# Performance work log

Measured on AMD Instinct MI355X. Metric: run time of the kernel, lower is better.

## Reference

```python
import jax, jax.numpy as jnp
import numpy as np

D_MODEL, N_LEVELS, N_HEADS, N_POINTS = 256, 4, 8, 4
HEAD_DIM = D_MODEL // N_HEADS
SPATIAL = np.array([[128, 128], [64, 64], [32, 32], [16, 16]], dtype=np.int64)
STARTS = np.concatenate([[0], np.cumsum(SPATIAL[:, 0] * SPATIAL[:, 1])[:-1]]).astype(np.int64)
N_TOK = int((SPATIAL[:, 0] * SPATIAL[:, 1]).sum())  # 21760
B, NQ = 2, 8192


def setup_inputs() -> dict:
    key = jax.random.key(0)
    ks = jax.random.split(key, 12)
    s = 1.0 / np.sqrt(D_MODEL)
    return {
        "query": jax.random.normal(ks[0], (B, NQ, D_MODEL), jnp.float32),
        "reference_points": jax.random.uniform(ks[1], (B, NQ, N_LEVELS, 2), jnp.float32),
        "input_flatten": jax.random.normal(ks[2], (B, N_TOK, D_MODEL), jnp.float32),
        "input_spatial_shapes": jnp.asarray(SPATIAL),
        "input_level_start_index": jnp.asarray(STARTS),
        "Wq": jax.random.normal(ks[3], (D_MODEL, D_MODEL), jnp.float32) * s,
        "bq": jnp.zeros((D_MODEL,), jnp.float32),
        "Wv": jax.random.normal(ks[4], (D_MODEL, D_MODEL), jnp.float32) * s,
        "bv": jnp.zeros((D_MODEL,), jnp.float32),
        "Wa": jax.random.normal(ks[5], (D_MODEL, N_HEADS * N_LEVELS * N_POINTS), jnp.float32) * s,
        "ba": jnp.zeros((N_HEADS * N_LEVELS * N_POINTS,), jnp.float32),
        "sampling_loc": jax.random.uniform(ks[6], (N_HEADS, N_LEVELS, N_POINTS, 2), jnp.float32, -0.1, 0.1),
        "Wo": jax.random.normal(ks[7], (D_MODEL, D_MODEL), jnp.float32) * s,
        "bo": jnp.zeros((D_MODEL,), jnp.float32),
    }


def _bilinear_sample(v_flat, grid, Hl, Wl):
    # v_flat: [B, H, Hl*Wl, Dh]; grid: [B, Nq, H, P, 2] in [-1, 1]
    b, nq, h, p, _ = grid.shape
    gx, gy = grid[..., 0], grid[..., 1]
    # align_corners=False pixel coordinates
    ix = ((gx + 1.0) * Wl - 1.0) * 0.5
    iy = ((gy + 1.0) * Hl - 1.0) * 0.5
    x0f, y0f = jnp.floor(ix), jnp.floor(iy)
    x0, y0 = x0f.astype(jnp.int32), y0f.astype(jnp.int32)
    x1, y1 = x0 + 1, y0 + 1
    wx1, wy1 = ix - x0f, iy - y0f
    wx0, wy0 = 1.0 - wx1, 1.0 - wy1

    def t(a):  # [B,Nq,H,P] -> [B,H,Nq*P]
        return a.transpose(0, 2, 1, 3).reshape(b, h, nq * p)

    def corner(yi, xi, w):
        valid = (xi >= 0) & (xi < Wl) & (yi >= 0) & (yi < Hl)
        idx = jnp.clip(yi, 0, Hl - 1) * Wl + jnp.clip(xi, 0, Wl - 1)
        g = jnp.take_along_axis(v_flat, t(idx)[..., None], axis=2)  # [B,H,Nq*P,Dh]
        return g * t(w * valid.astype(w.dtype))[..., None]

    out = (corner(y0, x0, wy0 * wx0) + corner(y0, x1, wy0 * wx1)
           + corner(y1, x0, wy1 * wx0) + corner(y1, x1, wy1 * wx1))
    return out.reshape(b, h, nq, p, -1)  # [B,H,Nq,P,Dh]


def reference(query, reference_points, input_flatten, input_spatial_shapes,
              input_level_start_index, Wq, bq, Wv, bv, Wa, ba, sampling_loc, Wo, bo):
    b, nq, c = query.shape
    h, L, p, _ = sampling_loc.shape
    dh = c // h
    q = query @ Wq + bq                                   # [B,Nq,C]
    attn = (q @ Wa + ba).reshape(b, nq, h, L, p)
    attn = jax.nn.softmax(attn, axis=-1)                  # softmax over points per level
    v = (input_flatten @ Wv + bv).reshape(b, -1, h, dh)   # [B,N,H,Dh]
    loc = reference_points[:, :, None, :, None, :] + sampling_loc[None, None]  # [B,Nq,H,L,P,2]
    grid = 2.0 * loc - 1.0
    shapes = np.asarray(input_spatial_shapes)
    starts = np.asarray(input_level_start_index)
    samples = []
    for lvl in range(L):
        Hl, Wl = int(shapes[lvl, 0]), int(shapes[lvl, 1])
        s0 = int(starts[lvl])
        vl = v[:, s0:s0 + Hl * Wl].transpose(0, 2, 1, 3)  # [B,H,Hl*Wl,Dh]
        samples.append(_bilinear_sample(vl, grid[:, :, :, lvl], Hl, Wl))
    samples = jnp.stack(samples, axis=3)                  # [B,H,Nq,L,P,Dh]
    out = jnp.einsum('bhnlpd,bnhlp->bnhd', samples, attn).reshape(b, nq, c)
    return out @ Wo + bo
```

## Files before the change

kernel.cpp:

```cpp
#include <hip/hip_runtime.h>
#include <hip/hip_bf16.h>

#define BATCH 2
#define NQ 8192
#define NTOK 21760

typedef __attribute__((ext_vector_type(4))) float f32x4;
typedef __attribute__((ext_vector_type(8))) short s16x8;

static __device__ __forceinline__ unsigned short f2bu(float x) {
    __hip_bfloat16 h = __float2bfloat16(x);
    return __builtin_bit_cast(unsigned short, h);
}
static __device__ __forceinline__ float blo(unsigned int u) { return __uint_as_float(u << 16); }
static __device__ __forceinline__ float bhi(unsigned int u) { return __uint_as_float(u & 0xffff0000u); }

__global__ void wqa_kernel(const float* __restrict__ Wq, const float* __restrict__ Wa,
                           const float* __restrict__ bq, const float* __restrict__ ba,
                           unsigned short* __restrict__ WqaT, float* __restrict__ bqa) {
    const int i = blockIdx.x;
    const int j = threadIdx.x;
    float acc = 0.f;
#pragma unroll 8
    for (int k = 0; k < 256; ++k) acc += Wq[i * 256 + k] * Wa[k * 128 + j];
    WqaT[j * 256 + i] = f2bu(acc);
    if (i == 0) {
        float b = ba[j];
#pragma unroll 8
        for (int k = 0; k < 256; ++k) b += bq[k] * Wa[k * 128 + j];
        bqa[j] = b;
    }
}

__global__ __launch_bounds__(256) void transpose_kernel(const float* __restrict__ Wv, const float* __restrict__ Wo,
                                                        unsigned short* __restrict__ WvT, unsigned short* __restrict__ WoT) {
    __shared__ float t[32][33];
    const int bid = blockIdx.x;
    const int mat = bid >> 6;
    const int tile = bid & 63;
    const int i0 = (tile >> 3) * 32, j0 = (tile & 7) * 32;
    const float* src = mat ? Wo : Wv;
    unsigned short* dst = mat ? WoT : WvT;
    const int tx = threadIdx.x & 31, ty = threadIdx.x >> 5;
#pragma unroll
    for (int r = 0; r < 4; ++r)
        t[ty + 8 * r][tx] = src[(i0 + ty + 8 * r) * 256 + j0 + tx];
    __syncthreads();
#pragma unroll
    for (int r = 0; r < 4; ++r)
        dst[(j0 + ty + 8 * r) * 256 + i0 + tx] = f2bu(t[tx][ty + 8 * r]);
}

template <int BM, int BN, int WRN, int WCN, bool AFP32, bool BF16OUT>
__global__ __launch_bounds__(256) void gemm_mfma(
    const void* __restrict__ Av, const unsigned short* __restrict__ Bt,
    const float* __restrict__ bias, void* __restrict__ Cv, int N) {
    constexpr int K = 256, NT = 4;
    constexpr int IM = BM / (WRN * 16);
    constexpr int JN = BN / (WCN * 16);
    constexpr int RA = BM / 32;
    constexpr int RB = BN / 32;
    __shared__ __align__(16) char As[BM * 128];
    __shared__ __align__(16) char Bs[BN * 128];
    const int tid = threadIdx.x;
    const int lane = tid & 63;
    const int wave = tid >> 6;
    const int wr = wave / WCN, wc = wave % WCN;
    const int bm = blockIdx.y * BM, bn = blockIdx.x * BN;
    const int srow = tid >> 3;
    const int skc = (tid & 7) * 8;

    f32x4 acc[IM][JN] = {};
    float4 af0[2][RA], af1[2][RA];
    s16x8 ab[2][RA], bb[2][RB];

    auto loadT = [&](int t, int buf) {
        const int k0 = t * 64;
#pragma unroll
        for (int r = 0; r < RA; ++r) {
            const int row = bm + srow + r * 32;
            if constexpr (AFP32) {
                const float* Af = (const float*)Av + (size_t)row * K + k0 + skc;
                af0[buf][r] = *(const float4*)Af;
                af1[buf][r] = *(const float4*)(Af + 4);
            } else {
                ab[buf][r] = *(const s16x8*)((const unsigned short*)Av + (size_t)row * K + k0 + skc);
            }
        }
#pragma unroll
        for (int r = 0; r < RB; ++r) {
            const int row = bn + srow + r * 32;
            bb[buf][r] = *(const s16x8*)(Bt + (size_t)row * K + k0 + skc);
        }
    };
    auto writeT = [&](int buf) {
#pragma unroll
        for (int r = 0; r < RA; ++r) {
            const int row = srow + r * 32;
            const int byte = (row * 128 + skc * 2) ^ ((row & 7) << 4);
            s16x8 av;
            if constexpr (AFP32) {
                const float4 f0 = af0[buf][r], f1 = af1[buf][r];
                av[0] = (short)f2bu(f0.x); av[1] = (short)f2bu(f0.y);
                av[2] = (short)f2bu(f0.z); av[3] = (short)f2bu(f0.w);
                av[4] = (short)f2bu(f1.x); av[5] = (short)f2bu(f1.y);
                av[6] = (short)f2bu(f1.z); av[7] = (short)f2bu(f1.w);
            } else {
                av = ab[buf][r];
            }
            *(s16x8*)(As + byte) = av;
        }
#pragma unroll
        for (int r = 0; r < RB; ++r) {
            const int row = srow + r * 32;
            const int byte = (row * 128 + skc * 2) ^ ((row & 7) << 4);
            *(s16x8*)(Bs + byte) = bb[buf][r];
        }
    };

    loadT(0, 0);
#pragma unroll
    for (int t = 0; t < NT; ++t) {
        if (t) __syncthreads();
        writeT(t & 1);
        if (t + 1 < NT) loadT(t + 1, (t + 1) & 1);
        __syncthreads();
#pragma unroll
        for (int f = 0; f < 2; ++f) {
            s16x8 a[IM], b[JN];
#pragma unroll
            for (int i = 0; i < IM; ++i) {
                const int arow = wr * (IM * 16) + i * 16 + (lane & 15);
                const int abyte = (arow * 128 + f * 64 + (lane >> 4) * 16) ^ ((arow & 7) << 4);
                a[i] = *(const s16x8*)(As + abyte);
            }
#pragma unroll
            for (int j = 0; j < JN; ++j) {
                const int brow = wc * (JN * 16) + j * 16 + (lane & 15);
                const int bbyte = (brow * 128 + f * 64 + (lane >> 4) * 16) ^ ((brow & 7) << 4);
                b[j] = *(const s16x8*)(Bs + bbyte);
            }
#pragma unroll
            for (int i = 0; i < IM; ++i)
#pragma unroll
                for (int j = 0; j < JN; ++j)
                    acc[i][j] = __builtin_amdgcn_mfma_f32_16x16x32_bf16(a[i], b[j], acc[i][j], 0, 0, 0);
        }
    }

#pragma unroll
    for (int i = 0; i < IM; ++i) {
        const int row0 = bm + wr * (IM * 16) + i * 16 + (lane >> 4) * 4;
#pragma unroll
        for (int j = 0; j < JN; ++j) {
            const int col = bn + wc * (JN * 16) + j * 16 + (lane & 15);
            const float bsv = bias[col];
#pragma unroll
            for (int q = 0; q < 4; ++q) {
                const float val = acc[i][j][q] + bsv;
                if constexpr (BF16OUT)
                    ((unsigned short*)Cv)[(size_t)(row0 + q) * N + col] = f2bu(val);
                else
                    ((float*)Cv)[(size_t)(row0 + q) * N + col] = val;
            }
        }
    }
}

__global__ __launch_bounds__(256) void sample_kernel(
    const float* __restrict__ refp, const float* __restrict__ sloc,
    const unsigned int* __restrict__ v,
    const float* __restrict__ logits,
    unsigned int* __restrict__ samp) {
    const int tid = threadIdx.x;
    const int q0 = blockIdx.x * 4;
    __shared__ int4 metaI[512];
    __shared__ float4 metaW[512];
    __shared__ float slc[256];
    __shared__ float lgs[512];
    __shared__ float rps[32];

    {
        const int l = (tid >> 3) & 3;
        slc[tid] = sloc[tid] * (float)(128 >> l) - 0.5f;
    }
    lgs[tid] = logits[(size_t)q0 * 128 + tid];
    lgs[tid + 256] = logits[(size_t)q0 * 128 + tid + 256];
    if (tid < 32) rps[tid] = refp[(size_t)q0 * 8 + tid];
    __syncthreads();

#pragma unroll
    for (int ss = 0; ss < 2; ++ss) {
        const int h = tid & 7;
        const int p = (tid >> 3) & 3;
        const int l = (tid >> 5) & 3;
        const int qi = (tid >> 7) + ss * 2;
        const int lp = l * 4 + p;
        const int bq = q0 + qi;
        const int b = bq >> 13;
        const int Wl = 128 >> l;
        const float lg = lgs[qi * 128 + h * 16 + lp];
        float m = fmaxf(lg, __shfl_xor(lg, 8));
        m = fmaxf(m, __shfl_xor(m, 16));
        const float e = __expf(lg - m);
        float sum = e + __shfl_xor(e, 8);
        sum += __shfl_xor(sum, 16);
        const float a = e / sum;
        const float fW = (float)Wl;
        const float ix = fmaf(rps[qi * 8 + l * 2 + 0], fW, slc[h * 32 + l * 8 + p * 2 + 0]);
        const float iy = fmaf(rps[qi * 8 + l * 2 + 1], fW, slc[h * 32 + l * 8 + p * 2 + 1]);
        const float xf = floorf(ix), yf = floorf(iy);
        const int x0 = (int)xf, y0 = (int)yf;
        const int x1 = x0 + 1, y1 = y0 + 1;
        float wx1 = ix - xf, wy1 = iy - yf;
        float wx0 = 1.f - wx1, wy0 = 1.f - wy1;
        wx0 = ((unsigned)x0 < (unsigned)Wl) ? wx0 : 0.f;
        wx1 = ((unsigned)x1 < (unsigned)Wl) ? wx1 : 0.f;
        wy0 = ((unsigned)y0 < (unsigned)Wl) ? wy0 * a : 0.f;
        wy1 = ((unsigned)y1 < (unsigned)Wl) ? wy1 * a : 0.f;
        const int x0c = min(max(x0, 0), Wl - 1);
        const int x1c = min(max(x1, 0), Wl - 1);
        const int y0c = min(max(y0, 0), Wl - 1);
        const int y1c = min(max(y1, 0), Wl - 1);
        const int SS = (65536 - (65536 >> (2 * l))) / 3;
        const int base = b * (NTOK * 128) + SS * 128 + h * 16;
        const int r0 = y0c * Wl, r1 = y1c * Wl;
        const int s = lp * 32 + qi * 8 + h;
        metaI[s] = make_int4(base + (r0 + x0c) * 128, base + (r0 + x1c) * 128,
                             base + (r1 + x0c) * 128, base + (r1 + x1c) * 128);
        metaW[s] = make_float4(wy0 * wx0, wy0 * wx1, wy1 * wx0, wy1 * wx1);
    }
    __syncthreads();

    const int qi = tid >> 6, h = (tid >> 3) & 7, c = tid & 7;
    const unsigned int* vp = v + c * 2;
    float a0 = 0.f, a1 = 0.f, a2 = 0.f, a3 = 0.f;
#pragma unroll
    for (int lp = 0; lp < 16; ++lp) {
        const int s = lp * 32 + qi * 8 + h;
        const int4 I = metaI[s];
        const float4 W = metaW[s];
        uint2 u;
        u = *(const uint2*)(vp + I.x);
        a0 = fmaf(blo(u.x), W.x, a0); a1 = fmaf(bhi(u.x), W.x, a1);
        a2 = fmaf(blo(u.y), W.x, a2); a3 = fmaf(bhi(u.y), W.x, a3);
        u = *(const uint2*)(vp + I.y);
        a0 = fmaf(blo(u.x), W.y, a0); a1 = fmaf(bhi(u.x), W.y, a1);
        a2 = fmaf(blo(u.y), W.y, a2); a3 = fmaf(bhi(u.y), W.y, a3);
        u = *(const uint2*)(vp + I.z);
        a0 = fmaf(blo(u.x), W.z, a0); a1 = fmaf(bhi(u.x), W.z, a1);
        a2 = fmaf(blo(u.y), W.z, a2); a3 = fmaf(bhi(u.y), W.z, a3);
        u = *(const uint2*)(vp + I.w);
        a0 = fmaf(blo(u.x), W.w, a0); a1 = fmaf(bhi(u.x), W.w, a1);
        a2 = fmaf(blo(u.y), W.w, a2); a3 = fmaf(bhi(u.y), W.w, a3);
    }
    const int bq = q0 + qi;
    uint2 o;
    o.x = (unsigned)f2bu(a0) | ((unsigned)f2bu(a1) << 16);
    o.y = (unsigned)f2bu(a2) | ((unsigned)f2bu(a3) << 16);
    *(uint2*)(samp + (size_t)bq * 128 + h * 16 + c * 2) = o;
}

extern "C" void kernel_launch(void* const* d_in, const int* in_sizes, int n_in,
                              void* d_out, int out_size, void* d_ws, size_t ws_size,
                              hipStream_t stream) {
    const float* query  = (const float*)d_in[0];
    const float* refp   = (const float*)d_in[1];
    const float* inflat = (const float*)d_in[2];
    const float* Wq = (const float*)d_in[5];
    const float* bq = (const float*)d_in[6];
    const float* Wv = (const float*)d_in[7];
    const float* bv = (const float*)d_in[8];
    const float* Wa = (const float*)d_in[9];
    const float* ba = (const float*)d_in[10];
    const float* sloc = (const float*)d_in[11];
    const float* Wo = (const float*)d_in[12];
    const float* bo = (const float*)d_in[13];
    float* out = (float*)d_out;

    char* ws = (char*)d_ws;
    unsigned short* WqaT = (unsigned short*)(ws + 0);
    float* bqa = (float*)(ws + (64u << 10));
    unsigned short* WvT = (unsigned short*)(ws + (128u << 10));
    unsigned short* WoT = (unsigned short*)(ws + (256u << 10));
    unsigned int* vbuf = (unsigned int*)(ws + (1u << 20));
    float* logits = (float*)(ws + (24u << 20));
    unsigned int* samp = (unsigned int*)(ws + (32u << 20));

    wqa_kernel<<<256, 128, 0, stream>>>(Wq, Wa, bq, ba, WqaT, bqa);
    transpose_kernel<<<128, 256, 0, stream>>>(Wv, Wo, WvT, WoT);
    gemm_mfma<128, 128, 2, 2, true, true><<<dim3(2, 340), 256, 0, stream>>>(inflat, WvT, bv, vbuf, 256);
    gemm_mfma<64, 64, 2, 2, true, false><<<dim3(2, 256), 256, 0, stream>>>(query, WqaT, bqa, logits, 128);
    sample_kernel<<<BATCH * NQ / 4, 256, 0, stream>>>(refp, sloc, (const unsigned int*)vbuf, logits, samp);
    gemm_mfma<64, 128, 1, 4, false, false><<<dim3(2, 256), 256, 0, stream>>>(samp, WoT, bo, out, 256);
}
```

Measured before the change: 206.8 us.

## Merge prep and projection kernels, restructure sampler with wider loads and prefetch

Merges the weight-prep kernels into one launch and fuses the value and query/logit projections into a single grouped GEMM launch, which cuts launch count and tail effects. The sampler now runs with 128 threads: each thread loads 16-byte bf16 chunks, prefetches the next sample's corners in software, keeps bilinear weights in fp16, and pads shared-memory metadata to avoid bank conflicts. The GEMMs now issue global loads before the shared-memory writes for better overlap. The trade-offs are lower weight precision and higher register pressure in the sampler.

New measurement: 242.7 us. 17.3% more time.

```diff
diff --git a/kernel.cpp b/kernel.cpp
--- a/kernel.cpp
+++ b/kernel.cpp
@@ -7,54 +7,174 @@
 
 typedef __attribute__((ext_vector_type(4))) float f32x4;
 typedef __attribute__((ext_vector_type(8))) short s16x8;
+typedef __attribute__((ext_vector_type(4))) _Float16 f16x4;
 
 static __device__ __forceinline__ unsigned short f2bu(float x) {
     __hip_bfloat16 h = __float2bfloat16(x);
     return __builtin_bit_cast(unsigned short, h);
 }
-static __device__ __forceinline__ float blo(unsigned int u) { return __uint_as_float(u << 16); }
-static __device__ __forceinline__ float bhi(unsigned int u) { return __uint_as_float(u & 0xffff0000u); }
-
-__global__ void wqa_kernel(const float* __restrict__ Wq, const float* __restrict__ Wa,
-                           const float* __restrict__ bq, const float* __restrict__ ba,
-                           unsigned short* __restrict__ WqaT, float* __restrict__ bqa) {
-    const int i = blockIdx.x;
-    const int j = threadIdx.x;
-    float acc = 0.f;
+
+__global__ __launch_bounds__(256) void prep_kernel(
+    const float* __restrict__ Wq, const float* __restrict__ Wa,
+    const float* __restrict__ bq, const float* __restrict__ ba,
+    const float* __restrict__ Wv, const float* __restrict__ Wo,
+    unsigned short* __restrict__ WqaT, float* __restrict__ bqa,
+    unsigned short* __restrict__ WvT, unsigned short* __restrict__ WoT) {
+    const int bid = blockIdx.x;
+    const int tid = threadIdx.x;
+    if (bid < 128) {
+        __shared__ float t[32][33];
+        const int mat = bid >> 6;
+        const int tile = bid & 63;
+        const int i0 = (tile >> 3) * 32, j0 = (tile & 7) * 32;
+        const float* src = mat ? Wo : Wv;
+        unsigned short* dst = mat ? WoT : WvT;
+        const int tx = tid & 31, ty = tid >> 5;
+#pragma unroll
+        for (int r = 0; r < 4; ++r)
+            t[ty + 8 * r][tx] = src[(i0 + ty + 8 * r) * 256 + j0 + tx];
+        __syncthreads();
+#pragma unroll
+        for (int r = 0; r < 4; ++r)
+            dst[(j0 + ty + 8 * r) * 256 + i0 + tx] = f2bu(t[tx][ty + 8 * r]);
+    } else {
+        __shared__ float red[256];
+        const int i = bid - 128;
+        const int j = tid & 127, kh = tid >> 7;
+        float acc = 0.f;
 #pragma unroll 8
-    for (int k = 0; k < 256; ++k) acc += Wq[i * 256 + k] * Wa[k * 128 + j];
-    WqaT[j * 256 + i] = f2bu(acc);
-    if (i == 0) {
-        float b = ba[j];
+        for (int k = kh * 128; k < kh * 128 + 128; ++k)
+            acc += Wq[i * 256 + k] * Wa[k * 128 + j];
+        red[tid] = acc;
+        __syncthreads();
+        if (kh == 0) {
+            WqaT[j * 256 + i] = f2bu(red[j] + red[j + 128]);
+            if (i == 0) {
+                float b = ba[j];
 #pragma unroll 8
-        for (int k = 0; k < 256; ++k) b += bq[k] * Wa[k * 128 + j];
-        bqa[j] = b;
-    }
-}
-
-__global__ __launch_bounds__(256) void transpose_kernel(const float* __restrict__ Wv, const float* __restrict__ Wo,
-                                                        unsigned short* __restrict__ WvT, unsigned short* __restrict__ WoT) {
-    __shared__ float t[32][33];
+                for (int k = 0; k < 256; ++k) b += bq[k] * Wa[k * 128 + j];
+                bqa[j] = b;
+            }
+        }
+    }
+}
+
+__global__ __launch_bounds__(256) void gemm_vlog(
+    const float* __restrict__ inflat, const unsigned short* __restrict__ WvT,
+    const float* __restrict__ bv, unsigned short* __restrict__ vbuf,
+    const float* __restrict__ query, const unsigned short* __restrict__ WqaT,
+    const float* __restrict__ bqa, float* __restrict__ logits) {
+    constexpr int K = 256, NT = 4, RA = 4, RB = 4, IM = 4, JN = 4;
+    __shared__ __align__(16) char As[128 * 128];
+    __shared__ __align__(16) char Bs[128 * 128];
     const int bid = blockIdx.x;
-    const int mat = bid >> 6;
-    const int tile = bid & 63;
-    const int i0 = (tile >> 3) * 32, j0 = (tile & 7) * 32;
-    const float* src = mat ? Wo : Wv;
-    unsigned short* dst = mat ? WoT : WvT;
-    const int tx = threadIdx.x & 31, ty = threadIdx.x >> 5;
-#pragma unroll
-    for (int r = 0; r < 4; ++r)
-        t[ty + 8 * r][tx] = src[(i0 + ty + 8 * r) * 256 + j0 + tx];
-    __syncthreads();
-#pragma unroll
-    for (int r = 0; r < 4; ++r)
-        dst[(j0 + ty + 8 * r) * 256 + i0 + tx] = f2bu(t[tx][ty + 8 * r]);
-}
-
-template <int BM, int BN, int WRN, int WCN, bool AFP32, bool BF16OUT>
-__global__ __launch_bounds__(256) void gemm_mfma(
-    const void* __restrict__ Av, const unsigned short* __restrict__ Bt,
-    const float* __restrict__ bias, void* __restrict__ Cv, int N) {
+    const float* A;
+    const unsigned short* Bt;
+    const float* bias;
+    int bm, bn, N;
+    bool b16;
+    if (bid < 680) {
+        A = inflat; Bt = WvT; bias = bv;
+        bm = (bid >> 1) * 128; bn = (bid & 1) * 128; N = 256; b16 = true;
+    } else {
+        A = query; Bt = WqaT; bias = bqa;
+        bm = (bid - 680) * 128; bn = 0; N = 128; b16 = false;
+    }
+    const int tid = threadIdx.x;
+    const int lane = tid & 63;
+    const int wave = tid >> 6;
+    const int wr = wave >> 1, wc = wave & 1;
+    const int srow = tid >> 3;
+    const int skc = (tid & 7) * 8;
+
+    f32x4 acc[IM][JN] = {};
+    float4 af0[2][RA], af1[2][RA];
+    s16x8 bb[2][RB];
+
+    auto loadT = [&](int t, int buf) {
+        const int k0 = t * 64;
+#pragma unroll
+        for (int r = 0; r < RA; ++r) {
+            const float* Af = A + (size_t)(bm + srow + r * 32) * K + k0 + skc;
+            af0[buf][r] = *(const float4*)Af;
+            af1[buf][r] = *(const float4*)(Af + 4);
+        }
+#pragma unroll
+        for (int r = 0; r < RB; ++r)
+            bb[buf][r] = *(const s16x8*)(Bt + (size_t)(bn + srow + r * 32) * K + k0 + skc);
+    };
+    auto writeT = [&](int buf) {
+#pragma unroll
+        for (int r = 0; r < RA; ++r) {
+            const int row = srow + r * 32;
+            const int byte = (row * 128 + skc * 2) ^ ((row & 7) << 4);
+            const float4 f0 = af0[buf][r], f1 = af1[buf][r];
+            s16x8 av;
+            av[0] = (short)f2bu(f0.x); av[1] = (short)f2bu(f0.y);
+            av[2] = (short)f2bu(f0.z); av[3] = (short)f2bu(f0.w);
+            av[4] = (short)f2bu(f1.x); av[5] = (short)f2bu(f1.y);
+            av[6] = (short)f2bu(f1.z); av[7] = (short)f2bu(f1.w);
+            *(s16x8*)(As + byte) = av;
+        }
+#pragma unroll
+        for (int r = 0; r < RB; ++r) {
+            const int row = srow + r * 32;
+            const int byte = (row * 128 + skc * 2) ^ ((row & 7) << 4);
+            *(s16x8*)(Bs + byte) = bb[buf][r];
+        }
+    };
+
+    loadT(0, 0);
+#pragma unroll
+    for (int t = 0; t < NT; ++t) {
+        if (t) __syncthreads();
+        if (t + 1 < NT) loadT(t + 1, (t + 1) & 1);
+        writeT(t & 1);
+        __syncthreads();
+#pragma unroll
+        for (int f = 0; f < 2; ++f) {
+            s16x8 a[IM], b[JN];
+#pragma unroll
+            for (int i = 0; i < IM; ++i) {
+                const int arow = wr * 64 + i * 16 + (lane & 15);
+                const int abyte = (arow * 128 + f * 64 + (lane >> 4) * 16) ^ ((arow & 7) << 4);
+                a[i] = *(const s16x8*)(As + abyte);
+            }
+#pragma unroll
+            for (int j = 0; j < JN; ++j) {
+                const int brow = wc * 64 + j * 16 + (lane & 15);
+                const int bbyte = (brow * 128 + f * 64 + (lane >> 4) * 16) ^ ((brow & 7) << 4);
+                b[j] = *(const s16x8*)(Bs + bbyte);
+            }
+#pragma unroll
+            for (int i = 0; i < IM; ++i)
+#pragma unroll
+                for (int j = 0; j < JN; ++j)
+                    acc[i][j] = __builtin_amdgcn_mfma_f32_16x16x32_bf16(a[i], b[j], acc[i][j], 0, 0, 0);
+        }
+    }
+
+#pragma unroll
+    for (int i = 0; i < IM; ++i) {
+        const int row0 = bm + wr * 64 + i * 16 + (lane >> 4) * 4;
+#pragma unroll
+        for (int j = 0; j < JN; ++j) {
+            const int col = bn + wc * 64 + j * 16 + (lane & 15);
+            const float bsv = bias[col];
+#pragma unroll
+            for (int q = 0; q < 4; ++q) {
+                const float val = acc[i][j][q] + bsv;
+                if (b16) vbuf[(size_t)(row0 + q) * N + col] = f2bu(val);
+                else logits[(size_t)(row0 + q) * N + col] = val;
+            }
+        }
+    }
+}
+
+template <int BM, int BN, int WRN, int WCN>
+__global__ __launch_bounds__(256) void gemm_out(
+    const unsigned short* __restrict__ Av, const unsigned short* __restrict__ Bt,
+    const float* __restrict__ bias, float* __restrict__ Cv, int N) {
     constexpr int K = 256, NT = 4;
     constexpr int IM = BM / (WRN * 16);
     constexpr int JN = BN / (WCN * 16);
@@ -71,50 +191,27 @@
     const int skc = (tid & 7) * 8;
 
     f32x4 acc[IM][JN] = {};
-    float4 af0[2][RA], af1[2][RA];
     s16x8 ab[2][RA], bb[2][RB];
 
     auto loadT = [&](int t, int buf) {
         const int k0 = t * 64;
 #pragma unroll
-        for (int r = 0; r < RA; ++r) {
-            const int row = bm + srow + r * 32;
-            if constexpr (AFP32) {
-                const float* Af = (const float*)Av + (size_t)row * K + k0 + skc;
-                af0[buf][r] = *(const float4*)Af;
-                af1[buf][r] = *(const float4*)(Af + 4);
-            } else {
-                ab[buf][r] = *(const s16x8*)((const unsigned short*)Av + (size_t)row * K + k0 + skc);
-            }
-        }
-#pragma unroll
-        for (int r = 0; r < RB; ++r) {
-            const int row = bn + srow + r * 32;
-            bb[buf][r] = *(const s16x8*)(Bt + (size_t)row * K + k0 + skc);
-        }
+        for (int r = 0; r < RA; ++r)
+            ab[buf][r] = *(const s16x8*)(Av + (size_t)(bm + srow + r * 32) * K + k0 + skc);
+#pragma unroll
+        for (int r = 0; r < RB; ++r)
+            bb[buf][r] = *(const s16x8*)(Bt + (size_t)(bn + srow + r * 32) * K + k0 + skc);
     };
     auto writeT = [&](int buf) {
 #pragma unroll
         for (int r = 0; r < RA; ++r) {
             const int row = srow + r * 32;
-            const int byte = (row * 128 + skc * 2) ^ ((row & 7) << 4);
-            s16x8 av;
-            if constexpr (AFP32) {
-                const float4 f0 = af0[buf][r], f1 = af1[buf][r];
-                av[0] = (short)f2bu(f0.x); av[1] = (short)f2bu(f0.y);
-                av[2] = (short)f2bu(f0.z); av[3] = (short)f2bu(f0.w);
-                av[4] = (short)f2bu(f1.x); av[5] = (short)f2bu(f1.y);
-                av[6] = (short)f2bu(f1.z); av[7] = (short)f2bu(f1.w);
-            } else {
-                av = ab[buf][r];
-            }
-            *(s16x8*)(As + byte) = av;
+            *(s16x8*)(As + ((row * 128 + skc * 2) ^ ((row & 7) << 4))) = ab[buf][r];
         }
 #pragma unroll
         for (int r = 0; r < RB; ++r) {
             const int row = srow + r * 32;
-            const int byte = (row * 128 + skc * 2) ^ ((row & 7) << 4);
-            *(s16x8*)(Bs + byte) = bb[buf][r];
+            *(s16x8*)(Bs + ((row * 128 + skc * 2) ^ ((row & 7) << 4))) = bb[buf][r];
         }
     };
 
@@ -122,8 +219,8 @@
 #pragma unroll
     for (int t = 0; t < NT; ++t) {
         if (t) __syncthreads();
+        if (t + 1 < NT) loadT(t + 1, (t + 1) & 1);
         writeT(t & 1);
-        if (t + 1 < NT) loadT(t + 1, (t + 1) & 1);
         __syncthreads();
 #pragma unroll
         for (int f = 0; f < 2; ++f) {
@@ -131,14 +228,12 @@
 #pragma unroll
             for (int i = 0; i < IM; ++i) {
                 const int arow = wr * (IM * 16) + i * 16 + (lane & 15);
-                const int abyte = (arow * 128 + f * 64 + (lane >> 4) * 16) ^ ((arow & 7) << 4);
-                a[i] = *(const s16x8*)(As + abyte);
+                a[i] = *(const s16x8*)(As + ((arow * 128 + f * 64 + (lane >> 4) * 16) ^ ((arow & 7) << 4)));
             }
 #pragma unroll
             for (int j = 0; j < JN; ++j) {
                 const int brow = wc * (JN * 16) + j * 16 + (lane & 15);
-                const int bbyte = (brow * 128 + f * 64 + (lane >> 4) * 16) ^ ((brow & 7) << 4);
-                b[j] = *(const s16x8*)(Bs + bbyte);
+                b[j] = *(const s16x8*)(Bs + ((brow * 128 + f * 64 + (lane >> 4) * 16) ^ ((brow & 7) << 4)));
             }
 #pragma unroll
             for (int i = 0; i < IM; ++i)
@@ -156,48 +251,45 @@
             const int col = bn + wc * (JN * 16) + j * 16 + (lane & 15);
             const float bsv = bias[col];
 #pragma unroll
-            for (int q = 0; q < 4; ++q) {
-                const float val = acc[i][j][q] + bsv;
-                if constexpr (BF16OUT)
-                    ((unsigned short*)Cv)[(size_t)(row0 + q) * N + col] = f2bu(val);
-                else
-                    ((float*)Cv)[(size_t)(row0 + q) * N + col] = val;
-            }
-        }
-    }
-}
-
-__global__ __launch_bounds__(256) void sample_kernel(
+            for (int q = 0; q < 4; ++q)
+                Cv[(size_t)(row0 + q) * N + col] = acc[i][j][q] + bsv;
+        }
+    }
+}
+
+__global__ __launch_bounds__(128) void sample_kernel(
     const float* __restrict__ refp, const float* __restrict__ sloc,
     const unsigned int* __restrict__ v,
     const float* __restrict__ logits,
     unsigned int* __restrict__ samp) {
     const int tid = threadIdx.x;
     const int q0 = blockIdx.x * 4;
-    __shared__ int4 metaI[512];
-    __shared__ float4 metaW[512];
+    __shared__ int4 mI[528];
+    __shared__ f16x4 mW[528];
     __shared__ float slc[256];
     __shared__ float lgs[512];
     __shared__ float rps[32];
 
-    {
-        const int l = (tid >> 3) & 3;
-        slc[tid] = sloc[tid] * (float)(128 >> l) - 0.5f;
-    }
-    lgs[tid] = logits[(size_t)q0 * 128 + tid];
-    lgs[tid + 256] = logits[(size_t)q0 * 128 + tid + 256];
+#pragma unroll
+    for (int r = 0; r < 2; ++r) {
+        const int t = tid + 128 * r;
+        const int l = (t >> 3) & 3;
+        slc[t] = sloc[t] * (float)(128 >> l) - 0.5f;
+    }
+#pragma unroll
+    for (int r = 0; r < 4; ++r)
+        lgs[tid + 128 * r] = logits[(size_t)q0 * 128 + tid + 128 * r];
     if (tid < 32) rps[tid] = refp[(size_t)q0 * 8 + tid];
     __syncthreads();
 
 #pragma unroll
-    for (int ss = 0; ss < 2; ++ss) {
+    for (int ss = 0; ss < 4; ++ss) {
         const int h = tid & 7;
         const int p = (tid >> 3) & 3;
-        const int l = (tid >> 5) & 3;
-        const int qi = (tid >> 7) + ss * 2;
+        const int l = tid >> 5;
+        const int qi = ss;
         const int lp = l * 4 + p;
-        const int bq = q0 + qi;
-        const int b = bq >> 13;
+        const int b = (q0 + qi) >> 13;
         const int Wl = 128 >> l;
         const float lg = lgs[qi * 128 + h * 16 + lp];
         float m = fmaxf(lg, __shfl_xor(lg, 8));
@@ -226,39 +318,62 @@
         const int base = b * (NTOK * 128) + SS * 128 + h * 16;
         const int r0 = y0c * Wl, r1 = y1c * Wl;
         const int s = lp * 32 + qi * 8 + h;
-        metaI[s] = make_int4(base + (r0 + x0c) * 128, base + (r0 + x1c) * 128,
-                             base + (r1 + x0c) * 128, base + (r1 + x1c) * 128);
-        metaW[s] = make_float4(wy0 * wx0, wy0 * wx1, wy1 * wx0, wy1 * wx1);
+        const int ixd = s + lp;
+        mI[ixd] = make_int4(base + (r0 + x0c) * 128, base + (r0 + x1c) * 128,
+                            base + (r1 + x0c) * 128, base + (r1 + x1c) * 128);
+        mW[ixd] = (f16x4){(_Float16)(wy0 * wx0), (_Float16)(wy0 * wx1),
+                          (_Float16)(wy1 * wx0), (_Float16)(wy1 * wx1)};
     }
     __syncthreads();
 
-    const int qi = tid >> 6, h = (tid >> 3) & 7, c = tid & 7;
-    const unsigned int* vp = v + c * 2;
+    const int qi = tid >> 5, h = (tid >> 2) & 7, c = tid & 3;
+    const int sbase = qi * 8 + h;
     float a0 = 0.f, a1 = 0.f, a2 = 0.f, a3 = 0.f;
+    float a4 = 0.f, a5 = 0.f, a6 = 0.f, a7 = 0.f;
+
+    auto fma4 = [&](const uint4& u, float w) {
+        a0 = fmaf(__uint_as_float(u.x << 16), w, a0);
+        a1 = fmaf(__uint_as_float(u.x), w, a1);
+        a2 = fmaf(__uint_as_float(u.y << 16), w, a2);
+        a3 = fmaf(__uint_as_float(u.y), w, a3);
+        a4 = fmaf(__uint_as_float(u.z << 16), w, a4);
+        a5 = fmaf(__uint_as_float(u.z), w, a5);
+        a6 = fmaf(__uint_as_float(u.w << 16), w, a6);
+        a7 = fmaf(__uint_as_float(u.w), w, a7);
+    };
+
+    int4 I = mI[sbase];
+    f16x4 Wh = mW[sbase];
+    uint4 u0 = *((const uint4*)(v + I.x) + c);
+    uint4 u1 = *((const uint4*)(v + I.y) + c);
+    uint4 u2 = *((const uint4*)(v + I.z) + c);
+    uint4 u3 = *((const uint4*)(v + I.w) + c);
 #pragma unroll
     for (int lp = 0; lp < 16; ++lp) {
-        const int s = lp * 32 + qi * 8 + h;
-        const int4 I = metaI[s];
-        const float4 W = metaW[s];
-        uint2 u;
-        u = *(const uint2*)(vp + I.x);
-        a0 = fmaf(blo(u.x), W.x, a0); a1 = fmaf(bhi(u.x), W.x, a1);
-        a2 = fmaf(blo(u.y), W.x, a2); a3 = fmaf(bhi(u.y), W.x, a3);
-        u = *(const uint2*)(vp + I.y);
-        a0 = fmaf(blo(u.x), W.y, a0); a1 = fmaf(bhi(u.x), W.y, a1);
-        a2 = fmaf(blo(u.y), W.y, a2); a3 = fmaf(bhi(u.y), W.y, a3);
-        u = *(const uint2*)(vp + I.z);
-        a0 = fmaf(blo(u.x), W.z, a0); a1 = fmaf(bhi(u.x), W.z, a1);
-        a2 = fmaf(blo(u.y), W.z, a2); a3 = fmaf(bhi(u.y), W.z, a3);
-        u = *(const uint2*)(vp + I.w);
-        a0 = fmaf(blo(u.x), W.w, a0); a1 = fmaf(bhi(u.x), W.w, a1);
-        a2 = fmaf(blo(u.y), W.w, a2); a3 = fmaf(bhi(u.y), W.w, a3);
-    }
-    const int bq = q0 + qi;
-    uint2 o;
+        int4 In;
+        f16x4 Wn;
+        uint4 n0, n1, n2, n3;
+        if (lp < 15) {
+            const int s = (lp + 1) * 32 + sbase;
+            In = mI[s + lp + 1];
+            Wn = mW[s + lp + 1];
+            n0 = *((const uint4*)(v + In.x) + c);
+            n1 = *((const uint4*)(v + In.y) + c);
+            n2 = *((const uint4*)(v + In.z) + c);
+            n3 = *((const uint4*)(v + In.w) + c);
+        }
+        fma4(u0, (float)Wh[0]);
+        fma4(u1, (float)Wh[1]);
+        fma4(u2, (float)Wh[2]);
+        fma4(u3, (float)Wh[3]);
+        if (lp < 15) { I = In; Wh = Wn; u0 = n0; u1 = n1; u2 = n2; u3 = n3; }
+    }
+    uint4 o;
     o.x = (unsigned)f2bu(a0) | ((unsigned)f2bu(a1) << 16);
     o.y = (unsigned)f2bu(a2) | ((unsigned)f2bu(a3) << 16);
-    *(uint2*)(samp + (size_t)bq * 128 + h * 16 + c * 2) = o;
+    o.z = (unsigned)f2bu(a4) | ((unsigned)f2bu(a5) << 16);
+    o.w = (unsigned)f2bu(a6) | ((unsigned)f2bu(a7) << 16);
+    *(uint4*)(samp + (size_t)(q0 + qi) * 128 + h * 16 + c * 4) = o;
 }
 
 extern "C" void kernel_launch(void* const* d_in, const int* in_sizes, int n_in,
@@ -283,14 +398,12 @@
     float* bqa = (float*)(ws + (64u << 10));
     unsigned short* WvT = (unsigned short*)(ws + (128u << 10));
     unsigned short* WoT = (unsigned short*)(ws + (256u << 10));
-    unsigned int* vbuf = (unsigned int*)(ws + (1u << 20));
+    unsigned short* vbuf = (unsigned short*)(ws + (1u << 20));
     float* logits = (float*)(ws + (24u << 20));
     unsigned int* samp = (unsigned int*)(ws + (32u << 20));
 
-    wqa_kernel<<<256, 128, 0, stream>>>(Wq, Wa, bq, ba, WqaT, bqa);
-    transpose_kernel<<<128, 256, 0, stream>>>(Wv, Wo, WvT, WoT);
-    gemm_mfma<128, 128, 2, 2, true, true><<<dim3(2, 340), 256, 0, stream>>>(inflat, WvT, bv, vbuf, 256);
-    gemm_mfma<64, 64, 2, 2, true, false><<<dim3(2, 256), 256, 0, stream>>>(query, WqaT, bqa, logits, 128);
-    sample_kernel<<<BATCH * NQ / 4, 256, 0, stream>>>(refp, sloc, (const unsigned int*)vbuf, logits, samp);
-    gemm_mfma<64, 128, 1, 4, false, false><<<dim3(2, 256), 256, 0, stream>>>(samp, WoT, bo, out, 256);
-}
+    prep_kernel<<<384, 256, 0, stream>>>(Wq, Wa, bq, ba, Wv, Wo, WqaT, bqa, WvT, WoT);
+    gemm_vlog<<<808, 256, 0, stream>>>(inflat, WvT, bv, vbuf, query, WqaT, bqa, logits);
+    sample_kernel<<<BATCH * NQ / 4, 128, 0, stream>>>(refp, sloc, (const unsigned int*)vbuf, logits, samp);
+    gemm_out<64, 128, 1, 4><<<dim3(2, 256), 256, 0, stream>>>((const unsigned short*)samp, WoT, bo, out, 256);
+}
```
